# Kernel optimization log

Measured on AMD Instinct MI355X. Metric: run time of the kernel, lower is better.

The kernel has to match this reference:

```python
import jax, jax.numpy as jnp
import numpy as np
from jax import lax

# Fixed dims from MSSMamba defaults
B_, L_, DM = 2, 8192, 256
NH, HP, NS = 4, 64, 8          # nheads, headdim, d_state
DIN = NH * HP                  # d_inner = 256
DPROJ = 2 * DIN + 2 * NS + NH  # 532


def setup_inputs() -> dict:
    key = jax.random.key(0)
    ks = jax.random.split(key, 16)
    f = lambda k, s, sc=1.0: jax.random.normal(k, s, jnp.float32) * sc
    inp = {
        'x_H': f(ks[0], (B_, L_, DM)),
        'x_V': f(ks[1], (B_, L_, DM)),
        'W_in_H': f(ks[2], (DM, 2 * DPROJ), 0.05),
        'W_in_V': f(ks[3], (DM, 2 * DPROJ), 0.05),
        'W_out_HF': f(ks[4], (DIN, DM), 0.05),
        'W_out_HB': f(ks[5], (DIN, DM), 0.05),
        'W_out_VF': f(ks[6], (DIN, DM), 0.05),
        'W_out_VB': f(ks[7], (DIN, DM), 0.05),
        'W_out': f(ks[8], (4 * DM, DM), 0.05),
    }
    for i, nm in enumerate(['HF', 'HB', 'VF', 'VB']):
        kd = jax.random.fold_in(ks[9], i)
        ka = jax.random.fold_in(ks[10], i)
        inp['dt_bias_' + nm] = f(kd, (NH,), 0.1)
        inp['A_log_' + nm] = jnp.log(jax.random.uniform(ka, (NH,), jnp.float32, 1.0, 16.0))
        inp['D_' + nm] = jnp.ones((NH,), jnp.float32)
    # per-batch permutation mapping vertical position -> horizontal position
    inp['v2h'] = jax.vmap(lambda k: jax.random.permutation(k, L_))(
        jax.random.split(ks[11], B_)).astype(jnp.int32)
    return inp


def _scan_dir(zxbcdt, dt_bias, A_log, D):
    # zxbcdt: [b, l, DPROJ] -> Mamba2-style selective scan, ngroups=1
    z = zxbcdt[..., :DIN].reshape(B_, L_, NH, HP)
    xBC = jax.nn.silu(zxbcdt[..., DIN:DIN + DIN + 2 * NS])
    x = xBC[..., :DIN].reshape(B_, L_, NH, HP)
    Bm = xBC[..., DIN:DIN + NS]      # [b, l, n]
    Cm = xBC[..., DIN + NS:]         # [b, l, n]
    dt = jax.nn.softplus(zxbcdt[..., -NH:] + dt_bias)  # [b, l, h]
    A = -jnp.exp(A_log)              # [h]
    dA = jnp.exp(dt * A)             # [b, l, h]
    dBx = jnp.einsum('blh,bln,blhp->blhpn', dt, Bm, x)  # [b,l,h,p,n]

    def step(state, inp):
        dA_t, dBx_t, C_t = inp
        state = dA_t[..., None, None] * state + dBx_t   # [b,h,p,n]
        y_t = jnp.einsum('bhpn,bn->bhp', state, C_t)
        return state, y_t

    init = jnp.zeros((B_, NH, HP, NS), dt.dtype)
    _, ys = lax.scan(step, init, (jnp.moveaxis(dA, 1, 0),
                                  jnp.moveaxis(dBx, 1, 0),
                                  jnp.moveaxis(Cm, 1, 0)))
    y = jnp.moveaxis(ys, 0, 1) + D[None, None, :, None] * x  # skip D*x
    y = y * jax.nn.silu(z)                                   # gate
    return y.reshape(B_, L_, DIN)


def reference(x_H, x_V, W_in_H, W_in_V,
              dt_bias_HF, dt_bias_HB, dt_bias_VF, dt_bias_VB,
              A_log_HF, A_log_HB, A_log_VF, A_log_VB,
              D_HF, D_HB, D_VF, D_VB,
              W_out_HF, W_out_HB, W_out_VF, W_out_VB,
              W_out, v2h):
    zx_HF, zx_HB = jnp.split(x_H @ W_in_H, 2, axis=-1)
    zx_VF, zx_VB = jnp.split(x_V @ W_in_V, 2, axis=-1)
    # note: source applies out_proj_HB to the HF branch (kept faithful)
    y_HF = _scan_dir(zx_HF, dt_bias_HF, A_log_HF, D_HF) @ W_out_HB
    y_HB = _scan_dir(zx_HB[:, ::-1], dt_bias_HB, A_log_HB, D_HB)[:, ::-1] @ W_out_HF
    y_VF = _scan_dir(zx_VF, dt_bias_VF, A_log_VF, D_VF) @ W_out_VB
    y_VB = _scan_dir(zx_VB[:, ::-1], dt_bias_VB, A_log_VB, D_VB)[:, ::-1] @ W_out_VF
    # remap vertical-ordered outputs to horizontal ordering (scatter by v2h)
    bidx = jnp.arange(B_)[:, None]
    y_VF = jnp.zeros_like(y_VF).at[bidx, v2h].set(y_VF)
    y_VB = jnp.zeros_like(y_VB).at[bidx, v2h].set(y_VB)
    cat = jnp.concatenate([y_HF, y_HB, y_VF, y_VB], axis=-1)  # [b, l, 4*d_model]
    return jax.nn.silu(cat) @ W_out
```

## Files before the change

kernel.cpp:

```cpp
#include <hip/hip_runtime.h>
#include <hip/hip_bf16.h>

#define B_N 2
#define L_N 8192
#define ROWS 16384
#define CHUNK 32
#define NCHUNK 256
#define NPAD 1152

typedef __bf16 bf16x8 __attribute__((ext_vector_type(8)));
typedef float f32x4 __attribute__((ext_vector_type(4)));

__device__ __forceinline__ float siluf(float v) {
  return v * __builtin_amdgcn_rcpf(1.f + __expf(-v));
}
__device__ __forceinline__ float softplusf_(float v) {
  return fmaxf(v, 0.f) + log1pf(__expf(-fabsf(v)));
}
__device__ __forceinline__ unsigned short f2bf(float v) {
  union { __bf16 b; unsigned short u; } x;
  x.b = (__bf16)v;
  return x.u;
}
__device__ __forceinline__ float bf2f(unsigned short u) {
  union { unsigned u; float f; } x; x.u = ((unsigned)u) << 16;
  return x.f;
}

__device__ __forceinline__ void gload_lds16(const unsigned short* g, unsigned short* l) {
  __builtin_amdgcn_global_load_lds(
      (const __attribute__((address_space(1))) unsigned int*)g,
      (__attribute__((address_space(3))) unsigned int*)l, 16, 0, 0);
}

struct P4 { const float* p[4]; };

__global__ void k_prep_all(const float* __restrict__ xH, const float* __restrict__ xV,
                           const float* __restrict__ WH, const float* __restrict__ WV,
                           P4 ws, const float* __restrict__ W_out, const int* __restrict__ v2h,
                           unsigned short* __restrict__ xbf, unsigned short* __restrict__ Wt_in,
                           unsigned short* __restrict__ Wt_dirs, unsigned short* __restrict__ Wt_fin,
                           int* __restrict__ inv) {
  int bid = blockIdx.x;
  int tid = threadIdx.x;
  if (bid < 8192) {
    int mat = bid >> 12;
    int i = (bid & 4095) * 256 + tid;
    const float* s = mat ? xV : xH;
    float4 v = ((const float4*)s)[i];
    ushort4 o;
    o.x = f2bf(v.x); o.y = f2bf(v.y); o.z = f2bf(v.z); o.w = f2bf(v.w);
    ((ushort4*)(xbf + (size_t)mat * ROWS * 256))[i] = o;
  } else if (bid < 10496) {
    int i = (bid - 8192) * 256 + tid;
    int z = i / (NPAD * 256);
    int rem = i - z * (NPAD * 256);
    int n = rem >> 8, k = rem & 255;
    const float* W = z ? WV : WH;
    int sl = n >= 544;
    int cc = n - (sl ? 544 : 0);
    float v = (cc < 532) ? W[(long)k * 1064 + sl * 532 + cc] : 0.f;
    Wt_in[i] = f2bf(v);
  } else if (bid < 11520) {
    int i = (bid - 10496) * 256 + tid;
    int d = i >> 16;
    int rem = i & 65535;
    int n = rem >> 8, k = rem & 255;
    Wt_dirs[i] = f2bf(ws.p[d][(long)k * 256 + n]);
  } else if (bid < 12544) {
    int i = (bid - 11520) * 256 + tid;
    int n = i >> 10, k = i & 1023;
    Wt_fin[i] = f2bf(W_out[(long)k * 256 + n]);
  } else {
    int m = (bid - 12544) * 256 + tid;
    if (m < ROWS) {
      int b = m >> 13;
      inv[b * L_N + v2h[m]] = m;
    }
  }
}

struct ScanConsts {
  const float* dt_bias[4];
  const float* A_log[4];
  const float* D[4];
};

__global__ __launch_bounds__(256) void k_dtfix(
    const float* __restrict__ xH, const float* __restrict__ xV,
    const float* __restrict__ WH, const float* __restrict__ WV,
    ScanConsts sc, float* __restrict__ dtv_arr, float* __restrict__ dA_arr) {
  __shared__ float xs[32][257];
  __shared__ float Wsm[8][260];
  const int mat = blockIdx.y;
  const float* x = mat ? xV : xH;
  const float* W = mat ? WV : WH;
  const int r0 = blockIdx.x * 32;
  for (int i = threadIdx.x; i < 2048; i += 256) {
    int c = i >> 8, k = i & 255;
    int sl = c >> 2, h = c & 3;
    Wsm[c][k] = W[(long)k * 1064 + sl * 532 + 528 + h];
  }
  for (int i = threadIdx.x; i < 32 * 64; i += 256) {
    int rl = i >> 6, kq = (i & 63) * 4;
    float4 v = *(const float4*)(x + (long)(r0 + rl) * 256 + kq);
    xs[rl][kq + 0] = v.x; xs[rl][kq + 1] = v.y; xs[rl][kq + 2] = v.z; xs[rl][kq + 3] = v.w;
  }
  __syncthreads();
  const int rl = threadIdx.x >> 3, c = threadIdx.x & 7;
  float s = 0.f;
  #pragma unroll 8
  for (int k = 0; k < 256; ++k) s = fmaf(xs[rl][k], Wsm[c][k], s);
  const int sl = c >> 2, h = c & 3;
  const int dir = mat * 2 + sl;
  float dtv = softplusf_(s + sc.dt_bias[dir][h]);
  float dAv = __expf(dtv * (-__expf(sc.A_log[dir][h])));
  long o = ((long)dir * 4 + h) * ROWS + (r0 + rl);
  dtv_arr[o] = dtv;
  dA_arr[o] = dAv;
}

struct EpiIn {
  unsigned short* zsil;
  unsigned short* xsil;
  unsigned short* bc;
};

__global__ __launch_bounds__(256) void k_gemm_in(
    const unsigned short* __restrict__ Abase, const unsigned short* __restrict__ Btbase,
    EpiIn ep) {
  __shared__ unsigned short As[128 * 32];
  __shared__ unsigned short Bs[128 * 32];
  __shared__ unsigned short trs[4][16 * 72];
  const int tid = threadIdx.x;
  const int lane = tid & 63;
  const int wid = tid >> 6;
  const int wm = wid & 1, wn = wid >> 1;
  const int q = lane >> 4, r = lane & 15;
  const int m0 = blockIdx.x * 128;
  const int n0 = blockIdx.y * 128;
  const int z = blockIdx.z;
  const unsigned short* A = Abase + (long)z * ROWS * 256;
  const unsigned short* Bt = Btbase + (long)z * NPAD * 256;

  f32x4 acc[4][4] = {};
  const int swr = (r >> 1) & 3;

  for (int kt = 0; kt < 256; kt += 32) {
    #pragma unroll
    for (int i = 0; i < 2; ++i) {
      int idx = i * 256 + tid;
      int row = idx >> 2;
      int ch = (idx & 3) ^ ((row >> 1) & 3);
      gload_lds16(A + (long)(m0 + row) * 256 + kt + ch * 8,
                  &As[(size_t)(i * 256 + wid * 64) * 8]);
    }
    #pragma unroll
    for (int i = 0; i < 2; ++i) {
      int idx = i * 256 + tid;
      int row = idx >> 2;
      int ch = (idx & 3) ^ ((row >> 1) & 3);
      gload_lds16(Bt + (long)(n0 + row) * 256 + kt + ch * 8,
                  &Bs[(size_t)(i * 256 + wid * 64) * 8]);
    }
    __syncthreads();
    bf16x8 af[4], bfr[4];
    #pragma unroll
    for (int mi = 0; mi < 4; ++mi)
      af[mi] = *(const bf16x8*)&As[((wm * 64 + mi * 16 + r) * 4 + (q ^ swr)) * 8];
    #pragma unroll
    for (int ni = 0; ni < 4; ++ni)
      bfr[ni] = *(const bf16x8*)&Bs[((wn * 64 + ni * 16 + r) * 4 + (q ^ swr)) * 8];
    #pragma unroll
    for (int mi = 0; mi < 4; ++mi)
      #pragma unroll
      for (int ni = 0; ni < 4; ++ni)
        acc[mi][ni] = __builtin_amdgcn_mfma_f32_16x16x32_bf16(af[mi], bfr[ni], acc[mi][ni], 0, 0, 0);
    __syncthreads();
  }

  unsigned short* tr = trs[wid];
  #pragma unroll
  for (int mi = 0; mi < 4; ++mi) {
    #pragma unroll
    for (int ni = 0; ni < 4; ++ni)
      #pragma unroll
      for (int j = 0; j < 4; ++j)
        tr[(q * 4 + j) * 72 + ni * 16 + r] = f2bf(siluf(acc[mi][ni][j]));
    asm volatile("s_waitcnt lgkmcnt(0)" ::: "memory");
    #pragma unroll
    for (int pass = 0; pass < 2; ++pass) {
      int rl = pass * 8 + (lane >> 3);
      int c8 = (lane & 7) * 8;
      bf16x8 v = *(const bf16x8*)&tr[rl * 72 + c8];
      int row = m0 + wm * 64 + mi * 16 + rl;
      int col = n0 + wn * 64 + c8;
      int sl = col >= 544;
      int cc = col - (sl ? 544 : 0);
      if (cc < 528) {
        int dir = z * 2 + sl;
        if (cc < 256)
          *(bf16x8*)(ep.zsil + ((long)dir * ROWS + row) * 256 + cc) = v;
        else if (cc < 512)
          *(bf16x8*)(ep.xsil + ((long)dir * ROWS + row) * 256 + cc - 256) = v;
        else
          *(bf16x8*)(ep.bc + ((long)dir * ROWS + row) * 16 + cc - 512) = v;
      }
    }
    asm volatile("s_waitcnt lgkmcnt(0)" ::: "memory");
  }
}

__global__ __launch_bounds__(256) void k_fuse(
    const unsigned short* __restrict__ ybf,
    const unsigned short* __restrict__ Wt_dirs,
    const unsigned short* __restrict__ Wt_fin,
    const int* __restrict__ inv,
    float* __restrict__ pbuf) {
  __shared__ unsigned short Tl[64][264];
  __shared__ unsigned short As1[64 * 32];
  __shared__ unsigned short Bs1[256 * 32];
  __shared__ int arow[64];
  const int tid = threadIdx.x;
  const int lane = tid & 63;
  const int wid = tid >> 6;
  const int q = lane >> 4, r = lane & 15;
  const int r0 = blockIdx.x * 64;
  const int pair = blockIdx.y;
  const int swr = (r >> 1) & 3;

  if (tid < 64) arow[tid] = pair ? inv[r0 + tid] : (r0 + tid);
  __syncthreads();

  f32x4 acc_o[4][4] = {};

  #pragma unroll
  for (int dd = 0; dd < 2; ++dd) {
    const int d = pair * 2 + dd;
    const unsigned short* yd = ybf + (long)d * ROWS * 256;
    const unsigned short* Wd = Wt_dirs + (long)d * 65536;

    f32x4 acc_t[4][4] = {};
    for (int kt = 0; kt < 256; kt += 32) {
      {
        int row = tid >> 2;
        int ch = (tid & 3) ^ ((row >> 1) & 3);
        gload_lds16(yd + (long)arow[row] * 256 + kt + ch * 8, &As1[(size_t)(wid * 64) * 8]);
      }
      #pragma unroll
      for (int i = 0; i < 4; ++i) {
        int idx = i * 256 + tid;
        int row = idx >> 2;
        int ch = (idx & 3) ^ ((row >> 1) & 3);
        gload_lds16(Wd + (long)row * 256 + kt + ch * 8,
                    &Bs1[(size_t)(i * 256 + wid * 64) * 8]);
      }
      __syncthreads();
      bf16x8 af[4], bfr[4];
      #pragma unroll
      for (int mi = 0; mi < 4; ++mi)
        af[mi] = *(const bf16x8*)&As1[((mi * 16 + r) * 4 + (q ^ swr)) * 8];
      #pragma unroll
      for (int ni = 0; ni < 4; ++ni)
        bfr[ni] = *(const bf16x8*)&Bs1[((wid * 64 + ni * 16 + r) * 4 + (q ^ swr)) * 8];
      #pragma unroll
      for (int mi = 0; mi < 4; ++mi)
        #pragma unroll
        for (int ni = 0; ni < 4; ++ni)
          acc_t[mi][ni] = __builtin_amdgcn_mfma_f32_16x16x32_bf16(af[mi], bfr[ni], acc_t[mi][ni], 0, 0, 0);
      __syncthreads();
    }
    #pragma unroll
    for (int mi = 0; mi < 4; ++mi)
      #pragma unroll
      for (int ni = 0; ni < 4; ++ni)
        #pragma unroll
        for (int j = 0; j < 4; ++j)
          Tl[mi * 16 + q * 4 + j][wid * 64 + ni * 16 + r] = f2bf(siluf(acc_t[mi][ni][j]));
    __syncthreads();
    for (int kt = 0; kt < 256; kt += 32) {
      #pragma unroll
      for (int i = 0; i < 4; ++i) {
        int idx = i * 256 + tid;
        int row = idx >> 2;
        int ch = (idx & 3) ^ ((row >> 1) & 3);
        gload_lds16(Wt_fin + (long)row * 1024 + d * 256 + kt + ch * 8,
                    &Bs1[(size_t)(i * 256 + wid * 64) * 8]);
      }
      __syncthreads();
      bf16x8 af[4], bfr[4];
      #pragma unroll
      for (int mi = 0; mi < 4; ++mi)
        af[mi] = *(const bf16x8*)&Tl[mi * 16 + r][kt + q * 8];
      #pragma unroll
      for (int ni = 0; ni < 4; ++ni)
        bfr[ni] = *(const bf16x8*)&Bs1[((wid * 64 + ni * 16 + r) * 4 + (q ^ swr)) * 8];
      #pragma unroll
      for (int mi = 0; mi < 4; ++mi)
        #pragma unroll
        for (int ni = 0; ni < 4; ++ni)
          acc_o[mi][ni] = __builtin_amdgcn_mfma_f32_16x16x32_bf16(af[mi], bfr[ni], acc_o[mi][ni], 0, 0, 0);
      __syncthreads();
    }
  }

  float* pout = pbuf + (long)pair * ROWS * 256;
  #pragma unroll
  for (int mi = 0; mi < 4; ++mi)
    #pragma unroll
    for (int j = 0; j < 4; ++j) {
      int row = r0 + mi * 16 + q * 4 + j;
      #pragma unroll
      for (int ni = 0; ni < 4; ++ni) {
        int col = wid * 64 + ni * 16 + r;
        pout[(long)row * 256 + col] = acc_o[mi][ni][j];
      }
    }
}

__global__ void k_red(const float* __restrict__ pbuf, float* __restrict__ out) {
  int i = blockIdx.x * 256 + threadIdx.x;
  float4 a = ((const float4*)pbuf)[i];
  float4 b = ((const float4*)(pbuf + (size_t)ROWS * 256))[i];
  float4 o;
  o.x = a.x + b.x; o.y = a.y + b.y; o.z = a.z + b.z; o.w = a.w + b.w;
  ((float4*)out)[i] = o;
}

struct ScanP {
  const unsigned short* xsil;
  const unsigned short* zsil;
  const unsigned short* bc;
  const float* dtv;
  const float* dA;
  const float* D[4];
};

__global__ __launch_bounds__(64) void k_scan1(ScanP sp, float* __restrict__ S,
                                              float* __restrict__ P) {
  __shared__ __align__(16) float Bst[CHUNK][8];
  __shared__ float dAs[CHUNK];
  const int p = threadIdx.x;
  const int c = blockIdx.x;
  const int bh = blockIdx.y;
  const int d = blockIdx.z;
  const int b = bh >> 2, h = bh & 3;
  const int rev = d & 1;
  const int t0 = c * CHUNK;
  if (p < CHUNK) {
    const int t = t0 + p;
    const int l = rev ? (L_N - 1 - t) : t;
    const int row = (b << 13) + l;
    uint4 bv = *(const uint4*)(sp.bc + ((long)d * ROWS + row) * 16);
    const unsigned short* bu = (const unsigned short*)&bv;
    float dtvv = sp.dtv[((long)d * 4 + h) * ROWS + row];
    dAs[p] = sp.dA[((long)d * 4 + h) * ROWS + row];
    #pragma unroll
    for (int n = 0; n < 8; ++n) Bst[p][n] = bf2f(bu[n]) * dtvv;
  }
  __syncthreads();

  float st[8] = {0, 0, 0, 0, 0, 0, 0, 0};
  float cumdA = 1.f;
  const int l0 = rev ? (L_N - 1 - t0) : t0;
  const unsigned short* xp = sp.xsil + ((long)d * ROWS + (b << 13) + l0) * 256 + h * 64 + p;
  const long stp = rev ? -256L : 256L;

  unsigned short xa[8], xb[8];
  #pragma unroll
  for (int j = 0; j < 8; ++j) xa[j] = xp[(long)j * stp];
  #pragma unroll
  for (int g = 0; g < 4; ++g) {
    if (g < 3) {
      #pragma unroll
      for (int j = 0; j < 8; ++j) xb[j] = xp[(long)((g + 1) * 8 + j) * stp];
    }
    #pragma unroll
    for (int j = 0; j < 8; ++j) {
      int s = g * 8 + j;
      float x = bf2f(xa[j]);
      float dA = dAs[s];
      f32x4 B0 = *(const f32x4*)&Bst[s][0];
      f32x4 B1 = *(const f32x4*)&Bst[s][4];
      cumdA *= dA;
      st[0] = fmaf(dA, st[0], x * B0[0]);
      st[1] = fmaf(dA, st[1], x * B0[1]);
      st[2] = fmaf(dA, st[2], x * B0[2]);
      st[3] = fmaf(dA, st[3], x * B0[3]);
      st[4] = fmaf(dA, st[4], x * B1[0]);
      st[5] = fmaf(dA, st[5], x * B1[1]);
      st[6] = fmaf(dA, st[6], x * B1[2]);
      st[7] = fmaf(dA, st[7], x * B1[3]);
    }
    #pragma unroll
    for (int j = 0; j < 8; ++j) xa[j] = xb[j];
  }
  float* Sp = S + ((((long)d * NCHUNK + c) * 8 + bh) * 64 + p) * 8;
  #pragma unroll
  for (int n = 0; n < 8; ++n) Sp[n] = st[n];
  if (p == 0) P[((long)d * NCHUNK + c) * 8 + bh] = cumdA;
}

__global__ __launch_bounds__(512) void k_scan2(const float* __restrict__ S,
                                               const float* __restrict__ P,
                                               float* __restrict__ carry) {
  __shared__ float Pl[NCHUNK];
  const int tid = threadIdx.x;
  const int dbh = blockIdx.x;
  const int d = dbh >> 3, bh = dbh & 7;
  if (tid < NCHUNK) Pl[tid] = P[((long)d * NCHUNK + tid) * 8 + bh];
  __syncthreads();
  float cy = 0.f;
  carry[(((long)d * NCHUNK + 0) * 8 + bh) * 512 + tid] = 0.f;
  #pragma unroll 8
  for (int c = 1; c < NCHUNK; ++c) {
    const float Sv = S[(((long)d * NCHUNK + (c - 1)) * 8 + bh) * 512 + tid];
    cy = fmaf(Pl[c - 1], cy, Sv);
    carry[(((long)d * NCHUNK + c) * 8 + bh) * 512 + tid] = cy;
  }
}

__global__ __launch_bounds__(64) void k_scan3(ScanP sp, const float* __restrict__ carry,
                                              unsigned short* __restrict__ ybf) {
  __shared__ __align__(16) float Bst[CHUNK][8];
  __shared__ __align__(16) float Cst[CHUNK][8];
  __shared__ float dAs[CHUNK];
  const int p = threadIdx.x;
  const int c = blockIdx.x;
  const int bh = blockIdx.y;
  const int d = blockIdx.z;
  const int b = bh >> 2, h = bh & 3;
  const int rev = d & 1;
  const float Dv = sp.D[d][h];
  const int t0 = c * CHUNK;
  if (p < CHUNK) {
    const int t = t0 + p;
    const int l = rev ? (L_N - 1 - t) : t;
    const int row = (b << 13) + l;
    const unsigned short* bp = sp.bc + ((long)d * ROWS + row) * 16;
    uint4 bv = *(const uint4*)bp;
    uint4 cv = *(const uint4*)(bp + 8);
    const unsigned short* bu = (const unsigned short*)&bv;
    const unsigned short* cu = (const unsigned short*)&cv;
    float dtvv = sp.dtv[((long)d * 4 + h) * ROWS + row];
    dAs[p] = sp.dA[((long)d * 4 + h) * ROWS + row];
    #pragma unroll
    for (int n = 0; n < 8; ++n) Bst[p][n] = bf2f(bu[n]) * dtvv;
    #pragma unroll
    for (int n = 0; n < 8; ++n) Cst[p][n] = bf2f(cu[n]);
  }
  __syncthreads();

  float st[8];
  {
    const float* cp = carry + ((((long)d * NCHUNK + c) * 8 + bh) * 64 + p) * 8;
    #pragma unroll
    for (int n = 0; n < 8; ++n) st[n] = cp[n];
  }

  const int l0 = rev ? (L_N - 1 - t0) : t0;
  const long base = (long)(b << 13) + l0;
  const unsigned short* xp = sp.xsil + ((long)d * ROWS + base) * 256 + h * 64 + p;
  const unsigned short* zp = sp.zsil + ((long)d * ROWS + base) * 256 + h * 64 + p;
  unsigned short* yp = ybf + ((long)d * ROWS + base) * 256 + h * 64 + p;
  const long stp = rev ? -256L : 256L;

  unsigned short xa[8], xb[8], za[8], zb[8];
  #pragma unroll
  for (int j = 0; j < 8; ++j) { xa[j] = xp[(long)j * stp]; za[j] = zp[(long)j * stp]; }
  #pragma unroll
  for (int g = 0; g < 4; ++g) {
    if (g < 3) {
      #pragma unroll
      for (int j = 0; j < 8; ++j) {
        xb[j] = xp[(long)((g + 1) * 8 + j) * stp];
        zb[j] = zp[(long)((g + 1) * 8 + j) * stp];
      }
    }
    #pragma unroll
    for (int j = 0; j < 8; ++j) {
      int s = g * 8 + j;
      float x = bf2f(xa[j]);
      float zv = bf2f(za[j]);
      float dA = dAs[s];
      f32x4 B0 = *(const f32x4*)&Bst[s][0];
      f32x4 B1 = *(const f32x4*)&Bst[s][4];
      f32x4 C0 = *(const f32x4*)&Cst[s][0];
      f32x4 C1 = *(const f32x4*)&Cst[s][4];
      st[0] = fmaf(dA, st[0], x * B0[0]);
      st[1] = fmaf(dA, st[1], x * B0[1]);
      st[2] = fmaf(dA, st[2], x * B0[2]);
      st[3] = fmaf(dA, st[3], x * B0[3]);
      st[4] = fmaf(dA, st[4], x * B1[0]);
      st[5] = fmaf(dA, st[5], x * B1[1]);
      st[6] = fmaf(dA, st[6], x * B1[2]);
      st[7] = fmaf(dA, st[7], x * B1[3]);
      float y01 = fmaf(st[1], C0[1], st[0] * C0[0]);
      float y23 = fmaf(st[3], C0[3], st[2] * C0[2]);
      float y45 = fmaf(st[5], C1[1], st[4] * C1[0]);
      float y67 = fmaf(st[7], C1[3], st[6] * C1[2]);
      float y = (y01 + y23) + (y45 + y67);
      y = fmaf(Dv, x, y) * zv;
      yp[(long)s * stp] = f2bf(y);
    }
    #pragma unroll
    for (int j = 0; j < 8; ++j) { xa[j] = xb[j]; za[j] = zb[j]; }
  }
}

extern "C" void kernel_launch(void* const* d_in, const int* in_sizes, int n_in,
                              void* d_out, int out_size, void* d_ws, size_t ws_size,
                              hipStream_t stream) {
  const float* x_H = (const float*)d_in[0];
  const float* x_V = (const float*)d_in[1];
  const float* W_in_H = (const float*)d_in[2];
  const float* W_in_V = (const float*)d_in[3];
  const float* W_out_HF = (const float*)d_in[4];
  const float* W_out_HB = (const float*)d_in[5];
  const float* W_out_VF = (const float*)d_in[6];
  const float* W_out_VB = (const float*)d_in[7];
  const float* W_out = (const float*)d_in[8];
  const float* dt_bias_HF = (const float*)d_in[9];
  const float* A_log_HF = (const float*)d_in[10];
  const float* D_HF = (const float*)d_in[11];
  const float* dt_bias_HB = (const float*)d_in[12];
  const float* A_log_HB = (const float*)d_in[13];
  const float* D_HB = (const float*)d_in[14];
  const float* dt_bias_VF = (const float*)d_in[15];
  const float* A_log_VF = (const float*)d_in[16];
  const float* D_VF = (const float*)d_in[17];
  const float* dt_bias_VB = (const float*)d_in[18];
  const float* A_log_VB = (const float*)d_in[19];
  const float* D_VB = (const float*)d_in[20];
  const int* v2h = (const int*)d_in[21];

  char* ws = (char*)d_ws;
  size_t off = 0;
  auto alloc = [&](size_t bytes) {
    void* pp = ws + off;
    off = (off + bytes + 255) & ~(size_t)255;
    return pp;
  };
  unsigned short* xbf = (unsigned short*)alloc((size_t)2 * ROWS * 256 * 2);
  unsigned short* Wt_in = (unsigned short*)alloc((size_t)2 * NPAD * 256 * 2);
  unsigned short* Wt_dirs = (unsigned short*)alloc((size_t)4 * 65536 * 2);
  unsigned short* Wt_fin = (unsigned short*)alloc((size_t)256 * 1024 * 2);
  unsigned short* zsil = (unsigned short*)alloc((size_t)4 * ROWS * 256 * 2);
  unsigned short* xsil = (unsigned short*)alloc((size_t)4 * ROWS * 256 * 2);
  unsigned short* bc = (unsigned short*)alloc((size_t)4 * ROWS * 16 * 2);
  float* dtv_arr = (float*)alloc((size_t)16 * ROWS * 4);
  float* dA_arr = (float*)alloc((size_t)16 * ROWS * 4);
  unsigned short* ybf = (unsigned short*)alloc((size_t)4 * ROWS * 256 * 2);
  float* S = (float*)alloc((size_t)4 * NCHUNK * 8 * 512 * 4);
  float* P = (float*)alloc((size_t)4 * NCHUNK * 8 * 4);
  float* carry = (float*)alloc((size_t)4 * NCHUNK * 8 * 512 * 4);
  int* inv = (int*)alloc((size_t)ROWS * 4);
  float* pbuf = (float*)alloc((size_t)2 * ROWS * 256 * 4);

  P4 wdirs;
  wdirs.p[0] = W_out_HB; wdirs.p[1] = W_out_HF; wdirs.p[2] = W_out_VB; wdirs.p[3] = W_out_VF;
  k_prep_all<<<12608, 256, 0, stream>>>(x_H, x_V, W_in_H, W_in_V, wdirs, W_out, v2h,
                                        xbf, Wt_in, Wt_dirs, Wt_fin, inv);

  ScanConsts sc;
  sc.dt_bias[0] = dt_bias_HF; sc.dt_bias[1] = dt_bias_HB;
  sc.dt_bias[2] = dt_bias_VF; sc.dt_bias[3] = dt_bias_VB;
  sc.A_log[0] = A_log_HF; sc.A_log[1] = A_log_HB;
  sc.A_log[2] = A_log_VF; sc.A_log[3] = A_log_VB;
  sc.D[0] = D_HF; sc.D[1] = D_HB; sc.D[2] = D_VF; sc.D[3] = D_VB;

  EpiIn ep; ep.zsil = zsil; ep.xsil = xsil; ep.bc = bc;

  k_gemm_in<<<dim3(ROWS / 128, NPAD / 128, 2), 256, 0, stream>>>(xbf, Wt_in, ep);
  k_dtfix<<<dim3(ROWS / 32, 2), 256, 0, stream>>>(x_H, x_V, W_in_H, W_in_V, sc, dtv_arr, dA_arr);

  ScanP sp;
  sp.xsil = xsil; sp.zsil = zsil; sp.bc = bc; sp.dtv = dtv_arr; sp.dA = dA_arr;
  sp.D[0] = D_HF; sp.D[1] = D_HB; sp.D[2] = D_VF; sp.D[3] = D_VB;

  k_scan1<<<dim3(NCHUNK, 8, 4), 64, 0, stream>>>(sp, S, P);
  k_scan2<<<32, 512, 0, stream>>>(S, P, carry);
  k_scan3<<<dim3(NCHUNK, 8, 4), 64, 0, stream>>>(sp, carry, ybf);

  k_fuse<<<dim3(ROWS / 64, 2), 256, 0, stream>>>(ybf, Wt_dirs, Wt_fin, inv, pbuf);
  k_red<<<ROWS * 256 / 4 / 256, 256, 0, stream>>>(pbuf, (float*)d_out);

  (void)in_sizes; (void)n_in; (void)out_size; (void)ws_size;
}
```

Measured before the change: 275.6 us.

## Split fuse kernel per direction and reduce outputs with float atomics

The fused output kernel now launches one block per direction instead of one per direction pair, which doubles the grid and halves the serial work per block. Partial outputs are accumulated directly into the zero-initialised output with atomicAdd, so the pbuf write and the separate reduction kernel are no longer needed. Zeroing the output is folded into the prep kernel. The trade-off is four atomic adds per output element, which can contend and makes the floating-point summation order nondeterministic.

```diff
diff --git a/kernel.cpp b/kernel.cpp
--- a/kernel.cpp
+++ b/kernel.cpp
@@ -40,7 +40,7 @@
                            P4 ws, const float* __restrict__ W_out, const int* __restrict__ v2h,
                            unsigned short* __restrict__ xbf, unsigned short* __restrict__ Wt_in,
                            unsigned short* __restrict__ Wt_dirs, unsigned short* __restrict__ Wt_fin,
-                           int* __restrict__ inv) {
+                           float* __restrict__ dout, int* __restrict__ inv) {
   int bid = blockIdx.x;
   int tid = threadIdx.x;
   if (bid < 8192) {
@@ -71,8 +71,12 @@
     int i = (bid - 11520) * 256 + tid;
     int n = i >> 10, k = i & 1023;
     Wt_fin[i] = f2bf(W_out[(long)k * 256 + n]);
+  } else if (bid < 16640) {
+    int i = (bid - 12544) * 256 + tid;
+    float4 z = {0.f, 0.f, 0.f, 0.f};
+    ((float4*)dout)[i] = z;
   } else {
-    int m = (bid - 12544) * 256 + tid;
+    int m = (bid - 16640) * 256 + tid;
     if (m < ROWS) {
       int b = m >> 13;
       inv[b * L_N + v2h[m]] = m;
@@ -216,7 +220,7 @@
     const unsigned short* __restrict__ Wt_dirs,
     const unsigned short* __restrict__ Wt_fin,
     const int* __restrict__ inv,
-    float* __restrict__ pbuf) {
+    float* __restrict__ out) {
   __shared__ unsigned short Tl[64][264];
   __shared__ unsigned short As1[64 * 32];
   __shared__ unsigned short Bs1[256 * 32];
@@ -226,85 +230,79 @@
   const int wid = tid >> 6;
   const int q = lane >> 4, r = lane & 15;
   const int r0 = blockIdx.x * 64;
-  const int pair = blockIdx.y;
+  const int d = blockIdx.y;
   const int swr = (r >> 1) & 3;
 
-  if (tid < 64) arow[tid] = pair ? inv[r0 + tid] : (r0 + tid);
+  if (tid < 64) arow[tid] = (d >= 2) ? inv[r0 + tid] : (r0 + tid);
   __syncthreads();
 
+  const unsigned short* yd = ybf + (long)d * ROWS * 256;
+  const unsigned short* Wd = Wt_dirs + (long)d * 65536;
+
+  f32x4 acc_t[4][4] = {};
+  for (int kt = 0; kt < 256; kt += 32) {
+    {
+      int row = tid >> 2;
+      int ch = (tid & 3) ^ ((row >> 1) & 3);
+      gload_lds16(yd + (long)arow[row] * 256 + kt + ch * 8, &As1[(size_t)(wid * 64) * 8]);
+    }
+    #pragma unroll
+    for (int i = 0; i < 4; ++i) {
+      int idx = i * 256 + tid;
+      int row = idx >> 2;
+      int ch = (idx & 3) ^ ((row >> 1) & 3);
+      gload_lds16(Wd + (long)row * 256 + kt + ch * 8,
+                  &Bs1[(size_t)(i * 256 + wid * 64) * 8]);
+    }
+    __syncthreads();
+    bf16x8 af[4], bfr[4];
+    #pragma unroll
+    for (int mi = 0; mi < 4; ++mi)
+      af[mi] = *(const bf16x8*)&As1[((mi * 16 + r) * 4 + (q ^ swr)) * 8];
+    #pragma unroll
+    for (int ni = 0; ni < 4; ++ni)
+      bfr[ni] = *(const bf16x8*)&Bs1[((wid * 64 + ni * 16 + r) * 4 + (q ^ swr)) * 8];
+    #pragma unroll
+    for (int mi = 0; mi < 4; ++mi)
+      #pragma unroll
+      for (int ni = 0; ni < 4; ++ni)
+        acc_t[mi][ni] = __builtin_amdgcn_mfma_f32_16x16x32_bf16(af[mi], bfr[ni], acc_t[mi][ni], 0, 0, 0);
+    __syncthreads();
+  }
+  #pragma unroll
+  for (int mi = 0; mi < 4; ++mi)
+    #pragma unroll
+    for (int ni = 0; ni < 4; ++ni)
+      #pragma unroll
+      for (int j = 0; j < 4; ++j)
+        Tl[mi * 16 + q * 4 + j][wid * 64 + ni * 16 + r] = f2bf(siluf(acc_t[mi][ni][j]));
+  __syncthreads();
   f32x4 acc_o[4][4] = {};
-
-  #pragma unroll
-  for (int dd = 0; dd < 2; ++dd) {
-    const int d = pair * 2 + dd;
-    const unsigned short* yd = ybf + (long)d * ROWS * 256;
-    const unsigned short* Wd = Wt_dirs + (long)d * 65536;
-
-    f32x4 acc_t[4][4] = {};
-    for (int kt = 0; kt < 256; kt += 32) {
-      {
-        int row = tid >> 2;
-        int ch = (tid & 3) ^ ((row >> 1) & 3);
-        gload_lds16(yd + (long)arow[row] * 256 + kt + ch * 8, &As1[(size_t)(wid * 64) * 8]);
-      }
-      #pragma unroll
-      for (int i = 0; i < 4; ++i) {
-        int idx = i * 256 + tid;
-        int row = idx >> 2;
-        int ch = (idx & 3) ^ ((row >> 1) & 3);
-        gload_lds16(Wd + (long)row * 256 + kt + ch * 8,
-                    &Bs1[(size_t)(i * 256 + wid * 64) * 8]);
-      }
-      __syncthreads();
-      bf16x8 af[4], bfr[4];
-      #pragma unroll
-      for (int mi = 0; mi < 4; ++mi)
-        af[mi] = *(const bf16x8*)&As1[((mi * 16 + r) * 4 + (q ^ swr)) * 8];
+  for (int kt = 0; kt < 256; kt += 32) {
+    #pragma unroll
+    for (int i = 0; i < 4; ++i) {
+      int idx = i * 256 + tid;
+      int row = idx >> 2;
+      int ch = (idx & 3) ^ ((row >> 1) & 3);
+      gload_lds16(Wt_fin + (long)row * 1024 + d * 256 + kt + ch * 8,
+                  &Bs1[(size_t)(i * 256 + wid * 64) * 8]);
+    }
+    __syncthreads();
+    bf16x8 af[4], bfr[4];
+    #pragma unroll
+    for (int mi = 0; mi < 4; ++mi)
+      af[mi] = *(const bf16x8*)&Tl[mi * 16 + r][kt + q * 8];
+    #pragma unroll
+    for (int ni = 0; ni < 4; ++ni)
+      bfr[ni] = *(const bf16x8*)&Bs1[((wid * 64 + ni * 16 + r) * 4 + (q ^ swr)) * 8];
+    #pragma unroll
+    for (int mi = 0; mi < 4; ++mi)
       #pragma unroll
       for (int ni = 0; ni < 4; ++ni)
-        bfr[ni] = *(const bf16x8*)&Bs1[((wid * 64 + ni * 16 + r) * 4 + (q ^ swr)) * 8];
-      #pragma unroll
-      for (int mi = 0; mi < 4; ++mi)
-        #pragma unroll
-        for (int ni = 0; ni < 4; ++ni)
-          acc_t[mi][ni] = __builtin_amdgcn_mfma_f32_16x16x32_bf16(af[mi], bfr[ni], acc_t[mi][ni], 0, 0, 0);
-      __syncthreads();
-    }
-    #pragma unroll
-    for (int mi = 0; mi < 4; ++mi)
-      #pragma unroll
-      for (int ni = 0; ni < 4; ++ni)
-        #pragma unroll
-        for (int j = 0; j < 4; ++j)
-          Tl[mi * 16 + q * 4 + j][wid * 64 + ni * 16 + r] = f2bf(siluf(acc_t[mi][ni][j]));
+        acc_o[mi][ni] = __builtin_amdgcn_mfma_f32_16x16x32_bf16(af[mi], bfr[ni], acc_o[mi][ni], 0, 0, 0);
     __syncthreads();
-    for (int kt = 0; kt < 256; kt += 32) {
-      #pragma unroll
-      for (int i = 0; i < 4; ++i) {
-        int idx = i * 256 + tid;
-        int row = idx >> 2;
-        int ch = (idx & 3) ^ ((row >> 1) & 3);
-        gload_lds16(Wt_fin + (long)row * 1024 + d * 256 + kt + ch * 8,
-                    &Bs1[(size_t)(i * 256 + wid * 64) * 8]);
-      }
-      __syncthreads();
-      bf16x8 af[4], bfr[4];
-      #pragma unroll
-      for (int mi = 0; mi < 4; ++mi)
-        af[mi] = *(const bf16x8*)&Tl[mi * 16 + r][kt + q * 8];
-      #pragma unroll
-      for (int ni = 0; ni < 4; ++ni)
-        bfr[ni] = *(const bf16x8*)&Bs1[((wid * 64 + ni * 16 + r) * 4 + (q ^ swr)) * 8];
-      #pragma unroll
-      for (int mi = 0; mi < 4; ++mi)
-        #pragma unroll
-        for (int ni = 0; ni < 4; ++ni)
-          acc_o[mi][ni] = __builtin_amdgcn_mfma_f32_16x16x32_bf16(af[mi], bfr[ni], acc_o[mi][ni], 0, 0, 0);
-      __syncthreads();
-    }
-  }
-
-  float* pout = pbuf + (long)pair * ROWS * 256;
+  }
+
   #pragma unroll
   for (int mi = 0; mi < 4; ++mi)
     #pragma unroll
@@ -313,18 +311,9 @@
       #pragma unroll
       for (int ni = 0; ni < 4; ++ni) {
         int col = wid * 64 + ni * 16 + r;
-        pout[(long)row * 256 + col] = acc_o[mi][ni][j];
+        atomicAdd(&out[(long)row * 256 + col], acc_o[mi][ni][j]);
       }
     }
-}
-
-__global__ void k_red(const float* __restrict__ pbuf, float* __restrict__ out) {
-  int i = blockIdx.x * 256 + threadIdx.x;
-  float4 a = ((const float4*)pbuf)[i];
-  float4 b = ((const float4*)(pbuf + (size_t)ROWS * 256))[i];
-  float4 o;
-  o.x = a.x + b.x; o.y = a.y + b.y; o.z = a.z + b.z; o.w = a.w + b.w;
-  ((float4*)out)[i] = o;
 }
 
 struct ScanP {
@@ -555,12 +544,11 @@
   float* P = (float*)alloc((size_t)4 * NCHUNK * 8 * 4);
   float* carry = (float*)alloc((size_t)4 * NCHUNK * 8 * 512 * 4);
   int* inv = (int*)alloc((size_t)ROWS * 4);
-  float* pbuf = (float*)alloc((size_t)2 * ROWS * 256 * 4);
 
   P4 wdirs;
   wdirs.p[0] = W_out_HB; wdirs.p[1] = W_out_HF; wdirs.p[2] = W_out_VB; wdirs.p[3] = W_out_VF;
-  k_prep_all<<<12608, 256, 0, stream>>>(x_H, x_V, W_in_H, W_in_V, wdirs, W_out, v2h,
-                                        xbf, Wt_in, Wt_dirs, Wt_fin, inv);
+  k_prep_all<<<16704, 256, 0, stream>>>(x_H, x_V, W_in_H, W_in_V, wdirs, W_out, v2h,
+                                        xbf, Wt_in, Wt_dirs, Wt_fin, (float*)d_out, inv);
 
   ScanConsts sc;
   sc.dt_bias[0] = dt_bias_HF; sc.dt_bias[1] = dt_bias_HB;
@@ -582,8 +570,7 @@
   k_scan2<<<32, 512, 0, stream>>>(S, P, carry);
   k_scan3<<<dim3(NCHUNK, 8, 4), 64, 0, stream>>>(sp, carry, ybf);
 
-  k_fuse<<<dim3(ROWS / 64, 2), 256, 0, stream>>>(ybf, Wt_dirs, Wt_fin, inv, pbuf);
-  k_red<<<ROWS * 256 / 4 / 256, 256, 0, stream>>>(pbuf, (float*)d_out);
+  k_fuse<<<dim3(ROWS / 64, 4), 256, 0, stream>>>(ybf, Wt_dirs, Wt_fin, inv, (float*)d_out);
 
   (void)in_sizes; (void)n_in; (void)out_size; (void)ws_size;
 }
```

After: 305.9 us. +11.0%, slower.
